# Kernel tuning notes

Measured on AMD Instinct MI355X. Metric: run time of the kernel, lower is better.

The kernel has to match this reference:

```python
import jax, jax.numpy as jnp
import numpy as np

NEG_INF = -jnp.inf


def setup_inputs() -> dict:
    B, T, D = 2, 512, 256
    key = jax.random.key(0)
    ks = jax.random.split(key, 12)
    inp = {
        'x': jax.random.normal(ks[0], (B, T, D), jnp.float32),
        'last_x': jnp.zeros((B, 1, D), jnp.float32),
        'last_num': jnp.zeros((B, 1, D), jnp.float32),
        'last_den': jnp.zeros((B, 1, D), jnp.float32),
        'time_decay': jax.random.normal(ks[1], (D,), jnp.float32) * 0.5,
        'time_first': jax.random.normal(ks[2], (D,), jnp.float32) * 0.5,
        'time_mix_k': jax.random.uniform(ks[3], (1, 1, D), jnp.float32),
        'time_mix_v': jax.random.uniform(ks[4], (1, 1, D), jnp.float32),
        'time_mix_r': jax.random.uniform(ks[5], (1, 1, D), jnp.float32),
        'Wk': jax.random.normal(ks[6], (D, D), jnp.float32) * 0.02,
        'Wv': jax.random.normal(ks[7], (D, D), jnp.float32) * 0.02,
        'Wr': jax.random.normal(ks[8], (D, D), jnp.float32) * 0.02,
        'Wo': jax.random.normal(ks[9], (D, D), jnp.float32) * 0.02,
    }
    return inp


def reference(x, last_x, last_num, last_den, time_decay, time_first,
              time_mix_k, time_mix_v, time_mix_r, Wk, Wv, Wr, Wo):
    B, T, D = x.shape

    # time_shift: prepend last_x, drop last step
    xs = jnp.concatenate([last_x, x[:, :-1, :]], axis=1)  # (B,T,D)

    k = (x * time_mix_k + xs * (1.0 - time_mix_k)) @ Wk.T
    v = (x * time_mix_v + xs * (1.0 - time_mix_v)) @ Wv.T
    r = (x * time_mix_r + xs * (1.0 - time_mix_r)) @ Wr.T
    sr = jax.nn.sigmoid(r)

    # --- run_wkv (quadratic exp-masked formulation, faithful to source) ---
    w = -jnp.exp(time_decay)                      # (D,)
    t = jnp.arange(T + 1, dtype=x.dtype)
    # wt[i, j] = j - i
    wt = t[None, :T] - t[:T, None]                # (T,T)
    tw = w[None, :] * t[1:, None]                 # (T,D): w * (j+1)
    twt = w[None, None, :] * wt[:, :, None]       # (T,T,D)
    # causal mask: -inf where j < i (strictly lower triangle, tril_(-1))
    ii = jnp.arange(T)
    mask = jnp.where(ii[:, None] > ii[None, :], NEG_INF, 0.0).astype(x.dtype)
    ktw = twt[None] + k[:, :, None, :] + mask[None, :, :, None]  # (B,T,T,D)
    etw = jnp.exp(tw)                             # (T,D)
    ektw = jnp.exp(ktw)                           # (B,T,T,D)
    num = etw[None] * last_num + jnp.einsum('bijd,bid->bjd', ektw, v)  # (B,T,D)
    den = etw[None] * last_den + ektw.sum(axis=1)                      # (B,T,D)
    num_prev = jnp.concatenate([last_num, num[:, :-1, :]], axis=1)
    den_prev = jnp.concatenate([last_den, den[:, :-1, :]], axis=1)
    euk = jnp.exp(time_first[None, None, :] + k)
    wkv = (num_prev + euk * v) / (den_prev + euk)
    # ----------------------------------------------------------------------

    out = (wkv * sr) @ Wo.T
    return (out, x[:, -1:, :], num[:, -1:, :], den[:, -1:, :])
```

## Files before the change

### kernel.cpp

```cpp
#include <hip/hip_runtime.h>

#define TT 512
#define DD 256
#define BB 2
#define MM (BB*TT)
#define LCH 16
#define NCH (TT/LCH)

__global__ __launch_bounds__(128)
void gemm_mix_t(const float* __restrict__ X, const float* __restrict__ Xlast,
                const float* __restrict__ W0, const float* __restrict__ W1,
                const float* __restrict__ W2,
                const float* __restrict__ mx0, const float* __restrict__ mx1,
                const float* __restrict__ mx2,
                float* __restrict__ O0, float* __restrict__ O1,
                float* __restrict__ O2)
{
    const int mat = blockIdx.z;
    const float* W  = (mat == 0) ? W0  : (mat == 1) ? W1  : W2;
    const float* mx = (mat == 0) ? mx0 : (mat == 1) ? mx1 : mx2;
    float*       O  = (mat == 0) ? O0  : (mat == 1) ? O1  : O2;

    const int n0  = blockIdx.x * 32;
    const int m0  = blockIdx.y * 64;
    const int b   = m0 / TT;
    const int t0  = m0 % TT;
    const int tid = threadIdx.x;

    const int cc = (tid & 15) * 4;
    const int r8 = tid >> 4;
    const int tm = tid >> 3;
    const int tn = tid & 7;

    __shared__ float As[64][68];
    __shared__ float Bs[64][36];

    float acc[4][4] = {};

    for (int k0 = 0; k0 < DD; k0 += 64) {
        #pragma unroll
        for (int i = 0; i < 8; ++i) {
            const int rr  = r8 + i * 8;
            const int row = m0 + rr;
            const float4 xc = *(const float4*)&X[row * DD + k0 + cc];
            float4 xp;
            if (t0 + rr == 0) xp = *(const float4*)&Xlast[b * DD + k0 + cc];
            else              xp = *(const float4*)&X[(row - 1) * DD + k0 + cc];
            const float4 mv = *(const float4*)&mx[k0 + cc];
            As[cc + 0][rr] = xp.x + (xc.x - xp.x) * mv.x;
            As[cc + 1][rr] = xp.y + (xc.y - xp.y) * mv.y;
            As[cc + 2][rr] = xp.z + (xc.z - xp.z) * mv.z;
            As[cc + 3][rr] = xp.w + (xc.w - xp.w) * mv.w;
        }
        #pragma unroll
        for (int i = 0; i < 4; ++i) {
            const int rr = r8 + i * 8;
            const float4 wv = *(const float4*)&W[(n0 + rr) * DD + k0 + cc];
            Bs[cc + 0][rr] = wv.x;
            Bs[cc + 1][rr] = wv.y;
            Bs[cc + 2][rr] = wv.z;
            Bs[cc + 3][rr] = wv.w;
        }
        __syncthreads();
        #pragma unroll
        for (int kk = 0; kk < 64; ++kk) {
            const float4 a4 = *(const float4*)&As[kk][tm * 4];
            const float4 b4 = *(const float4*)&Bs[kk][tn * 4];
            const float am[4] = {a4.x, a4.y, a4.z, a4.w};
            const float bn[4] = {b4.x, b4.y, b4.z, b4.w};
            #pragma unroll
            for (int i = 0; i < 4; ++i)
                #pragma unroll
                for (int j = 0; j < 4; ++j)
                    acc[i][j] = fmaf(am[i], bn[j], acc[i][j]);
        }
        __syncthreads();
    }

    #pragma unroll
    for (int j = 0; j < 4; ++j) {
        const float4 o = make_float4(acc[0][j], acc[1][j], acc[2][j], acc[3][j]);
        *(float4*)&O[(size_t)(b * DD + n0 + tn * 4 + j) * TT + t0 + tm * 4] = o;
    }
}

__global__ __launch_bounds__(256)
void wkv_scan(const float* __restrict__ kT, const float* __restrict__ vT,
              const float* __restrict__ rT, const float* __restrict__ x,
              const float* __restrict__ last_num, const float* __restrict__ last_den,
              const float* __restrict__ time_decay, const float* __restrict__ time_first,
              float* __restrict__ yT, float* __restrict__ out)
{
    const int tid  = threadIdx.x;
    const int ch   = blockIdx.x * 8 + (tid >> 5);
    const int lane = tid & 31;
    const int b    = ch >> 8;
    const int d    = ch & (DD - 1);

    const float w  = -__expf(time_decay[d]);
    const float ew = __expf(w);
    const float eu = __expf(time_first[d]);

    const size_t base = (size_t)ch * TT + lane * LCH;
    float k_[LCH], v_[LCH], r_[LCH];
    #pragma unroll
    for (int i = 0; i < 4; ++i) {
        *(float4*)&k_[4 * i] = *(const float4*)(kT + base + 4 * i);
        *(float4*)&v_[4 * i] = *(const float4*)(vT + base + 4 * i);
        *(float4*)&r_[4 * i] = *(const float4*)(rT + base + 4 * i);
    }

    float ek[LCH], ekv[LCH], sr[LCH];
    #pragma unroll
    for (int i = 0; i < LCH; ++i) {
        ek[i]  = __expf(k_[i]);
        ekv[i] = ek[i] * v_[i];
        sr[i]  = __builtin_amdgcn_rcpf(1.0f + __expf(-r_[i]));
    }

    float A = __expf(w * (float)LCH);
    float Bn = 0.0f, Bd = 0.0f;
    #pragma unroll
    for (int i = 0; i < LCH; ++i) {
        Bn = fmaf(ew, Bn, ekv[i]);
        Bd = fmaf(ew, Bd, ek[i]);
    }

    #pragma unroll
    for (int s = 1; s < 32; s <<= 1) {
        const float Ax  = __shfl_up(A, s, 32);
        const float Bnx = __shfl_up(Bn, s, 32);
        const float Bdx = __shfl_up(Bd, s, 32);
        if (lane >= s) {
            Bn = fmaf(A, Bnx, Bn);
            Bd = fmaf(A, Bdx, Bd);
            A *= Ax;
        }
    }

    float Aex  = __shfl_up(A, 1, 32);
    float Bnex = __shfl_up(Bn, 1, 32);
    float Bdex = __shfl_up(Bd, 1, 32);
    if (lane == 0) { Aex = 1.0f; Bnex = 0.0f; Bdex = 0.0f; }
    float sn = fmaf(Aex, last_num[ch], Bnex);
    float sd = fmaf(Aex, last_den[ch], Bdex);

    float y_[LCH];
    #pragma unroll
    for (int i = 0; i < LCH; ++i) {
        const float euk = eu * ek[i];
        const float wkv = (sn + eu * ekv[i]) * __builtin_amdgcn_rcpf(sd + euk);
        y_[i] = wkv * sr[i];
        sn = fmaf(ew, sn, ekv[i]);
        sd = fmaf(ew, sd, ek[i]);
    }
    #pragma unroll
    for (int i = 0; i < 4; ++i)
        *(float4*)(yT + base + 4 * i) = *(const float4*)&y_[4 * i];

    if (lane == 31) {
        out[MM * DD + BB * DD + ch]     = sn;
        out[MM * DD + 2 * BB * DD + ch] = sd;
    }
    if (lane == 0)
        out[MM * DD + ch] = x[(b * TT + TT - 1) * DD + d];
}

__global__ __launch_bounds__(64)
void gemm_out(const float* __restrict__ yT, const float* __restrict__ Wo,
              float* __restrict__ O)
{
    const int n0  = blockIdx.x * 32;
    const int m0  = blockIdx.y * 32;
    const int b   = m0 >> 9;
    const int t0  = m0 & (TT - 1);
    const int tid = threadIdx.x;

    __shared__ float As[64][36];
    __shared__ float Bs[64][36];

    const int tm = tid >> 3;
    const int tn = tid & 7;

    float acc[4][4] = {};

    for (int k0 = 0; k0 < DD; k0 += 64) {
        {
            const int mq = (tid & 7) * 4;
            #pragma unroll
            for (int i = 0; i < 8; ++i) {
                const int kk = (tid >> 3) + i * 8;
                *(float4*)&As[kk][mq] =
                    *(const float4*)&yT[(size_t)(b * DD + k0 + kk) * TT + t0 + mq];
            }
        }
        {
            const int cc = (tid & 15) * 4;
            #pragma unroll
            for (int i = 0; i < 8; ++i) {
                const int rr = (tid >> 4) + i * 4;
                const float4 wv = *(const float4*)&Wo[(n0 + rr) * DD + k0 + cc];
                Bs[cc + 0][rr] = wv.x;
                Bs[cc + 1][rr] = wv.y;
                Bs[cc + 2][rr] = wv.z;
                Bs[cc + 3][rr] = wv.w;
            }
        }
        __syncthreads();
        #pragma unroll
        for (int kk = 0; kk < 64; ++kk) {
            const float4 a4 = *(const float4*)&As[kk][tm * 4];
            const float4 b4 = *(const float4*)&Bs[kk][tn * 4];
            const float am[4] = {a4.x, a4.y, a4.z, a4.w};
            const float bn[4] = {b4.x, b4.y, b4.z, b4.w};
            #pragma unroll
            for (int i = 0; i < 4; ++i)
                #pragma unroll
                for (int j = 0; j < 4; ++j)
                    acc[i][j] = fmaf(am[i], bn[j], acc[i][j]);
        }
        __syncthreads();
    }

    #pragma unroll
    for (int i = 0; i < 4; ++i) {
        const float4 o = make_float4(acc[i][0], acc[i][1], acc[i][2], acc[i][3]);
        *(float4*)&O[(size_t)(m0 + tm * 4 + i) * DD + n0 + tn * 4] = o;
    }
}

extern "C" void kernel_launch(void* const* d_in, const int* in_sizes, int n_in,
                              void* d_out, int out_size, void* d_ws, size_t ws_size,
                              hipStream_t stream)
{
    const float* x    = (const float*)d_in[0];
    const float* lx   = (const float*)d_in[1];
    const float* lnum = (const float*)d_in[2];
    const float* lden = (const float*)d_in[3];
    const float* td   = (const float*)d_in[4];
    const float* tf   = (const float*)d_in[5];
    const float* mk   = (const float*)d_in[6];
    const float* mv   = (const float*)d_in[7];
    const float* mr   = (const float*)d_in[8];
    const float* Wk   = (const float*)d_in[9];
    const float* Wv   = (const float*)d_in[10];
    const float* Wr   = (const float*)d_in[11];
    const float* Wo   = (const float*)d_in[12];
    float* out = (float*)d_out;

    float* kT = (float*)d_ws;
    float* vT = kT + MM * DD;
    float* rT = vT + MM * DD;
    float* yT = rT + MM * DD;

    gemm_mix_t<<<dim3(8, 16, 3), 128, 0, stream>>>(
        x, lx, Wk, Wv, Wr, mk, mv, mr, kT, vT, rT);

    wkv_scan<<<dim3(64), 256, 0, stream>>>(
        kT, vT, rT, x, lnum, lden, td, tf, yT, out);

    gemm_out<<<dim3(8, 32), 64, 0, stream>>>(yT, Wo, out);
}
```

Baseline: 110.3 us.

## Double-buffer GEMM tiles with register prefetch and widen the WKV scan to 64 lanes

Both GEMM kernels now use double-buffered shared-memory tiles, prefetching the next K chunk into registers while the current one is computed, which removes one barrier per iteration. Blocks grow to 256 threads: the mix GEMM uses 64x64 tiles and the output GEMM gives each thread a 2x2 tile. The WKV scan uses full 64-lane wavefronts with 8-element chunks per lane and twice as many blocks, aiming for more parallelism and occupancy. The costs are a longer shuffle scan, fewer blocks in the mix GEMM, and lower per-thread compute density in the output GEMM.

```diff
diff --git a/kernel.cpp b/kernel.cpp
--- a/kernel.cpp
+++ b/kernel.cpp
@@ -4,10 +4,10 @@
 #define DD 256
 #define BB 2
 #define MM (BB*TT)
-#define LCH 16
+#define LCH 8
 #define NCH (TT/LCH)
 
-__global__ __launch_bounds__(128)
+__global__ __launch_bounds__(256)
 void gemm_mix_t(const float* __restrict__ X, const float* __restrict__ Xlast,
                 const float* __restrict__ W0, const float* __restrict__ W1,
                 const float* __restrict__ W2,
@@ -21,51 +21,71 @@
     const float* mx = (mat == 0) ? mx0 : (mat == 1) ? mx1 : mx2;
     float*       O  = (mat == 0) ? O0  : (mat == 1) ? O1  : O2;
 
-    const int n0  = blockIdx.x * 32;
+    const int n0  = blockIdx.x * 64;
     const int m0  = blockIdx.y * 64;
     const int b   = m0 / TT;
     const int t0  = m0 % TT;
     const int tid = threadIdx.x;
 
-    const int cc = (tid & 15) * 4;
-    const int r8 = tid >> 4;
-    const int tm = tid >> 3;
-    const int tn = tid & 7;
-
-    __shared__ float As[64][68];
-    __shared__ float Bs[64][36];
-
-    float acc[4][4] = {};
-
-    for (int k0 = 0; k0 < DD; k0 += 64) {
-        #pragma unroll
-        for (int i = 0; i < 8; ++i) {
-            const int rr  = r8 + i * 8;
+    const int cc = (tid & 7) * 4;
+    const int r8 = tid >> 3;
+    const int tm = tid >> 4;
+    const int tn = tid & 15;
+
+    __shared__ float As[2][32][68];
+    __shared__ float Bs[2][32][68];
+
+    float4 a0, a1, b0, b1;
+
+    auto load_chunk = [&](int k0) {
+        const float4 mv = *(const float4*)&mx[k0 + cc];
+        {
+            const int rr  = r8;
             const int row = m0 + rr;
-            const float4 xc = *(const float4*)&X[row * DD + k0 + cc];
+            const float4 xc = *(const float4*)&X[(size_t)row * DD + k0 + cc];
             float4 xp;
             if (t0 + rr == 0) xp = *(const float4*)&Xlast[b * DD + k0 + cc];
-            else              xp = *(const float4*)&X[(row - 1) * DD + k0 + cc];
-            const float4 mv = *(const float4*)&mx[k0 + cc];
-            As[cc + 0][rr] = xp.x + (xc.x - xp.x) * mv.x;
-            As[cc + 1][rr] = xp.y + (xc.y - xp.y) * mv.y;
-            As[cc + 2][rr] = xp.z + (xc.z - xp.z) * mv.z;
-            As[cc + 3][rr] = xp.w + (xc.w - xp.w) * mv.w;
-        }
-        #pragma unroll
-        for (int i = 0; i < 4; ++i) {
-            const int rr = r8 + i * 8;
-            const float4 wv = *(const float4*)&W[(n0 + rr) * DD + k0 + cc];
-            Bs[cc + 0][rr] = wv.x;
-            Bs[cc + 1][rr] = wv.y;
-            Bs[cc + 2][rr] = wv.z;
-            Bs[cc + 3][rr] = wv.w;
-        }
+            else              xp = *(const float4*)&X[(size_t)(row - 1) * DD + k0 + cc];
+            a0.x = xp.x + (xc.x - xp.x) * mv.x;
+            a0.y = xp.y + (xc.y - xp.y) * mv.y;
+            a0.z = xp.z + (xc.z - xp.z) * mv.z;
+            a0.w = xp.w + (xc.w - xp.w) * mv.w;
+            b0 = *(const float4*)&W[(size_t)(n0 + rr) * DD + k0 + cc];
+        }
+        {
+            const int rr  = r8 + 32;
+            const int row = m0 + rr;
+            const float4 xc = *(const float4*)&X[(size_t)row * DD + k0 + cc];
+            float4 xp;
+            if (t0 + rr == 0) xp = *(const float4*)&Xlast[b * DD + k0 + cc];
+            else              xp = *(const float4*)&X[(size_t)(row - 1) * DD + k0 + cc];
+            a1.x = xp.x + (xc.x - xp.x) * mv.x;
+            a1.y = xp.y + (xc.y - xp.y) * mv.y;
+            a1.z = xp.z + (xc.z - xp.z) * mv.z;
+            a1.w = xp.w + (xc.w - xp.w) * mv.w;
+            b1 = *(const float4*)&W[(size_t)(n0 + rr) * DD + k0 + cc];
+        }
+    };
+
+    float acc[4][4] = {};
+    load_chunk(0);
+
+    for (int c = 0; c < 8; ++c) {
+        const int buf = c & 1;
+        As[buf][cc + 0][r8]      = a0.x; As[buf][cc + 1][r8]      = a0.y;
+        As[buf][cc + 2][r8]      = a0.z; As[buf][cc + 3][r8]      = a0.w;
+        As[buf][cc + 0][r8 + 32] = a1.x; As[buf][cc + 1][r8 + 32] = a1.y;
+        As[buf][cc + 2][r8 + 32] = a1.z; As[buf][cc + 3][r8 + 32] = a1.w;
+        Bs[buf][cc + 0][r8]      = b0.x; Bs[buf][cc + 1][r8]      = b0.y;
+        Bs[buf][cc + 2][r8]      = b0.z; Bs[buf][cc + 3][r8]      = b0.w;
+        Bs[buf][cc + 0][r8 + 32] = b1.x; Bs[buf][cc + 1][r8 + 32] = b1.y;
+        Bs[buf][cc + 2][r8 + 32] = b1.z; Bs[buf][cc + 3][r8 + 32] = b1.w;
+        if (c < 7) load_chunk((c + 1) * 32);
         __syncthreads();
         #pragma unroll
-        for (int kk = 0; kk < 64; ++kk) {
-            const float4 a4 = *(const float4*)&As[kk][tm * 4];
-            const float4 b4 = *(const float4*)&Bs[kk][tn * 4];
+        for (int kk = 0; kk < 32; ++kk) {
+            const float4 a4 = *(const float4*)&As[buf][kk][tm * 4];
+            const float4 b4 = *(const float4*)&Bs[buf][kk][tn * 4];
             const float am[4] = {a4.x, a4.y, a4.z, a4.w};
             const float bn[4] = {b4.x, b4.y, b4.z, b4.w};
             #pragma unroll
@@ -74,7 +94,6 @@
                 for (int j = 0; j < 4; ++j)
                     acc[i][j] = fmaf(am[i], bn[j], acc[i][j]);
         }
-        __syncthreads();
     }
 
     #pragma unroll
@@ -92,8 +111,8 @@
               float* __restrict__ yT, float* __restrict__ out)
 {
     const int tid  = threadIdx.x;
-    const int ch   = blockIdx.x * 8 + (tid >> 5);
-    const int lane = tid & 31;
+    const int ch   = blockIdx.x * 4 + (tid >> 6);
+    const int lane = tid & 63;
     const int b    = ch >> 8;
     const int d    = ch & (DD - 1);
 
@@ -104,7 +123,7 @@
     const size_t base = (size_t)ch * TT + lane * LCH;
     float k_[LCH], v_[LCH], r_[LCH];
     #pragma unroll
-    for (int i = 0; i < 4; ++i) {
+    for (int i = 0; i < LCH / 4; ++i) {
         *(float4*)&k_[4 * i] = *(const float4*)(kT + base + 4 * i);
         *(float4*)&v_[4 * i] = *(const float4*)(vT + base + 4 * i);
         *(float4*)&r_[4 * i] = *(const float4*)(rT + base + 4 * i);
@@ -127,10 +146,10 @@
     }
 
     #pragma unroll
-    for (int s = 1; s < 32; s <<= 1) {
-        const float Ax  = __shfl_up(A, s, 32);
-        const float Bnx = __shfl_up(Bn, s, 32);
-        const float Bdx = __shfl_up(Bd, s, 32);
+    for (int s = 1; s < 64; s <<= 1) {
+        const float Ax  = __shfl_up(A, s, 64);
+        const float Bnx = __shfl_up(Bn, s, 64);
+        const float Bdx = __shfl_up(Bd, s, 64);
         if (lane >= s) {
             Bn = fmaf(A, Bnx, Bn);
             Bd = fmaf(A, Bdx, Bd);
@@ -138,9 +157,9 @@
         }
     }
 
-    float Aex  = __shfl_up(A, 1, 32);
-    float Bnex = __shfl_up(Bn, 1, 32);
-    float Bdex = __shfl_up(Bd, 1, 32);
+    float Aex  = __shfl_up(A, 1, 64);
+    float Bnex = __shfl_up(Bn, 1, 64);
+    float Bdex = __shfl_up(Bd, 1, 64);
     if (lane == 0) { Aex = 1.0f; Bnex = 0.0f; Bdex = 0.0f; }
     float sn = fmaf(Aex, last_num[ch], Bnex);
     float sd = fmaf(Aex, last_den[ch], Bdex);
@@ -155,10 +174,10 @@
         sd = fmaf(ew, sd, ek[i]);
     }
     #pragma unroll
-    for (int i = 0; i < 4; ++i)
+    for (int i = 0; i < LCH / 4; ++i)
         *(float4*)(yT + base + 4 * i) = *(const float4*)&y_[4 * i];
 
-    if (lane == 31) {
+    if (lane == 63) {
         out[MM * DD + BB * DD + ch]     = sn;
         out[MM * DD + 2 * BB * DD + ch] = sd;
     }
@@ -166,7 +185,7 @@
         out[MM * DD + ch] = x[(b * TT + TT - 1) * DD + d];
 }
 
-__global__ __launch_bounds__(64)
+__global__ __launch_bounds__(256)
 void gemm_out(const float* __restrict__ yT, const float* __restrict__ Wo,
               float* __restrict__ O)
 {
@@ -176,56 +195,53 @@
     const int t0  = m0 & (TT - 1);
     const int tid = threadIdx.x;
 
-    __shared__ float As[64][36];
-    __shared__ float Bs[64][36];
-
-    const int tm = tid >> 3;
-    const int tn = tid & 7;
-
-    float acc[4][4] = {};
-
-    for (int k0 = 0; k0 < DD; k0 += 64) {
-        {
-            const int mq = (tid & 7) * 4;
-            #pragma unroll
-            for (int i = 0; i < 8; ++i) {
-                const int kk = (tid >> 3) + i * 8;
-                *(float4*)&As[kk][mq] =
-                    *(const float4*)&yT[(size_t)(b * DD + k0 + kk) * TT + t0 + mq];
-            }
-        }
-        {
-            const int cc = (tid & 15) * 4;
-            #pragma unroll
-            for (int i = 0; i < 8; ++i) {
-                const int rr = (tid >> 4) + i * 4;
-                const float4 wv = *(const float4*)&Wo[(n0 + rr) * DD + k0 + cc];
-                Bs[cc + 0][rr] = wv.x;
-                Bs[cc + 1][rr] = wv.y;
-                Bs[cc + 2][rr] = wv.z;
-                Bs[cc + 3][rr] = wv.w;
-            }
-        }
+    __shared__ float As[2][64][36];
+    __shared__ float Bs[2][64][36];
+
+    const int tm = tid >> 4;
+    const int tn = tid & 15;
+
+    const int kq  = tid >> 3;
+    const int mq  = (tid & 7) * 4;
+    const int cc  = (tid & 15) * 4;
+    const int r16 = tid >> 4;
+
+    float4 av0, av1, wv0, wv1;
+    auto load_chunk = [&](int k0) {
+        av0 = *(const float4*)&yT[(size_t)(b * DD + k0 + kq) * TT + t0 + mq];
+        av1 = *(const float4*)&yT[(size_t)(b * DD + k0 + kq + 32) * TT + t0 + mq];
+        wv0 = *(const float4*)&Wo[(size_t)(n0 + r16) * DD + k0 + cc];
+        wv1 = *(const float4*)&Wo[(size_t)(n0 + r16 + 16) * DD + k0 + cc];
+    };
+
+    float acc[2][2] = {};
+    load_chunk(0);
+
+    for (int c = 0; c < 4; ++c) {
+        const int buf = c & 1;
+        *(float4*)&As[buf][kq][mq]      = av0;
+        *(float4*)&As[buf][kq + 32][mq] = av1;
+        Bs[buf][cc + 0][r16]      = wv0.x; Bs[buf][cc + 1][r16]      = wv0.y;
+        Bs[buf][cc + 2][r16]      = wv0.z; Bs[buf][cc + 3][r16]      = wv0.w;
+        Bs[buf][cc + 0][r16 + 16] = wv1.x; Bs[buf][cc + 1][r16 + 16] = wv1.y;
+        Bs[buf][cc + 2][r16 + 16] = wv1.z; Bs[buf][cc + 3][r16 + 16] = wv1.w;
+        if (c < 3) load_chunk((c + 1) * 64);
         __syncthreads();
         #pragma unroll
         for (int kk = 0; kk < 64; ++kk) {
-            const float4 a4 = *(const float4*)&As[kk][tm * 4];
-            const float4 b4 = *(const float4*)&Bs[kk][tn * 4];
-            const float am[4] = {a4.x, a4.y, a4.z, a4.w};
-            const float bn[4] = {b4.x, b4.y, b4.z, b4.w};
-            #pragma unroll
-            for (int i = 0; i < 4; ++i)
-                #pragma unroll
-                for (int j = 0; j < 4; ++j)
-                    acc[i][j] = fmaf(am[i], bn[j], acc[i][j]);
-        }
-        __syncthreads();
-    }
-
-    #pragma unroll
-    for (int i = 0; i < 4; ++i) {
-        const float4 o = make_float4(acc[i][0], acc[i][1], acc[i][2], acc[i][3]);
-        *(float4*)&O[(size_t)(m0 + tm * 4 + i) * DD + n0 + tn * 4] = o;
+            const float2 a2 = *(const float2*)&As[buf][kk][tm * 2];
+            const float2 b2 = *(const float2*)&Bs[buf][kk][tn * 2];
+            acc[0][0] = fmaf(a2.x, b2.x, acc[0][0]);
+            acc[0][1] = fmaf(a2.x, b2.y, acc[0][1]);
+            acc[1][0] = fmaf(a2.y, b2.x, acc[1][0]);
+            acc[1][1] = fmaf(a2.y, b2.y, acc[1][1]);
+        }
+    }
+
+    #pragma unroll
+    for (int i = 0; i < 2; ++i) {
+        const float2 o = make_float2(acc[i][0], acc[i][1]);
+        *(float2*)&O[(size_t)(m0 + tm * 2 + i) * DD + n0 + tn * 2] = o;
     }
 }
 
@@ -253,11 +269,11 @@
     float* rT = vT + MM * DD;
     float* yT = rT + MM * DD;
 
-    gemm_mix_t<<<dim3(8, 16, 3), 128, 0, stream>>>(
+    gemm_mix_t<<<dim3(4, 16, 3), 256, 0, stream>>>(
         x, lx, Wk, Wv, Wr, mk, mv, mr, kT, vT, rT);
 
-    wkv_scan<<<dim3(64), 256, 0, stream>>>(
+    wkv_scan<<<dim3(128), 256, 0, stream>>>(
         kT, vT, rT, x, lnum, lden, td, tf, yT, out);
 
-    gemm_out<<<dim3(8, 32), 64, 0, stream>>>(yT, Wo, out);
-}
+    gemm_out<<<dim3(8, 32), 256, 0, stream>>>(yT, Wo, out);
+}
```

Measured after the change: 102.2 us. 7.3% less time.

## Use single-wave blocks, split-K and finer scan chunks to spread work across CUs

Applied to the files above, without the earlier changes.

The mix GEMM now uses one 64-lane wave per block with 32x32 tiles and double-buffered shared memory. It prefetches the next K chunk into registers and drops the block barriers, which works because a single wave executes in lockstep. The output GEMM splits K across two waves and reduces their partial sums through shared memory. The WKV scan uses 8-element chunks with a full 64-lane wave scan, which gives four times as many blocks. Together these raise the number of blocks in flight on a small problem and cut barrier stalls, at the cost of more shuffle steps and an extra reduction pass.

```diff
diff --git a/kernel.cpp b/kernel.cpp
--- a/kernel.cpp
+++ b/kernel.cpp
@@ -4,10 +4,9 @@
 #define DD 256
 #define BB 2
 #define MM (BB*TT)
-#define LCH 16
-#define NCH (TT/LCH)
-
-__global__ __launch_bounds__(128)
+#define LCH 8
+
+__global__ __launch_bounds__(64)
 void gemm_mix_t(const float* __restrict__ X, const float* __restrict__ Xlast,
                 const float* __restrict__ W0, const float* __restrict__ W1,
                 const float* __restrict__ W2,
@@ -21,51 +20,58 @@
     const float* mx = (mat == 0) ? mx0 : (mat == 1) ? mx1 : mx2;
     float*       O  = (mat == 0) ? O0  : (mat == 1) ? O1  : O2;
 
-    const int n0  = blockIdx.x * 32;
-    const int m0  = blockIdx.y * 64;
-    const int b   = m0 / TT;
-    const int t0  = m0 % TT;
-    const int tid = threadIdx.x;
-
-    const int cc = (tid & 15) * 4;
-    const int r8 = tid >> 4;
-    const int tm = tid >> 3;
-    const int tn = tid & 7;
-
-    __shared__ float As[64][68];
-    __shared__ float Bs[64][36];
-
-    float acc[4][4] = {};
-
-    for (int k0 = 0; k0 < DD; k0 += 64) {
-        #pragma unroll
-        for (int i = 0; i < 8; ++i) {
-            const int rr  = r8 + i * 8;
+    const int n0   = blockIdx.x * 32;
+    const int m0   = blockIdx.y * 32;
+    const int b    = m0 / TT;
+    const int t0   = m0 % TT;
+    const int lane = threadIdx.x;
+
+    const int cc = (lane & 7) * 4;
+    const int g  = lane >> 3;
+    const int tm = lane >> 3;
+    const int tn = lane & 7;
+
+    __shared__ float As[2][32][36];
+    __shared__ float Bs[2][32][36];
+
+    float4 a[4], w4[4];
+
+    auto load_chunk = [&](int k0) {
+        const float4 mv = *(const float4*)&mx[k0 + cc];
+        #pragma unroll
+        for (int i = 0; i < 4; ++i) {
+            const int rr  = g + 8 * i;
             const int row = m0 + rr;
-            const float4 xc = *(const float4*)&X[row * DD + k0 + cc];
+            const float4 xc = *(const float4*)&X[(size_t)row * DD + k0 + cc];
             float4 xp;
             if (t0 + rr == 0) xp = *(const float4*)&Xlast[b * DD + k0 + cc];
-            else              xp = *(const float4*)&X[(row - 1) * DD + k0 + cc];
-            const float4 mv = *(const float4*)&mx[k0 + cc];
-            As[cc + 0][rr] = xp.x + (xc.x - xp.x) * mv.x;
-            As[cc + 1][rr] = xp.y + (xc.y - xp.y) * mv.y;
-            As[cc + 2][rr] = xp.z + (xc.z - xp.z) * mv.z;
-            As[cc + 3][rr] = xp.w + (xc.w - xp.w) * mv.w;
-        }
-        #pragma unroll
-        for (int i = 0; i < 4; ++i) {
-            const int rr = r8 + i * 8;
-            const float4 wv = *(const float4*)&W[(n0 + rr) * DD + k0 + cc];
-            Bs[cc + 0][rr] = wv.x;
-            Bs[cc + 1][rr] = wv.y;
-            Bs[cc + 2][rr] = wv.z;
-            Bs[cc + 3][rr] = wv.w;
-        }
-        __syncthreads();
-        #pragma unroll
-        for (int kk = 0; kk < 64; ++kk) {
-            const float4 a4 = *(const float4*)&As[kk][tm * 4];
-            const float4 b4 = *(const float4*)&Bs[kk][tn * 4];
+            else              xp = *(const float4*)&X[(size_t)(row - 1) * DD + k0 + cc];
+            a[i].x = xp.x + (xc.x - xp.x) * mv.x;
+            a[i].y = xp.y + (xc.y - xp.y) * mv.y;
+            a[i].z = xp.z + (xc.z - xp.z) * mv.z;
+            a[i].w = xp.w + (xc.w - xp.w) * mv.w;
+            w4[i] = *(const float4*)&W[(size_t)(n0 + rr) * DD + k0 + cc];
+        }
+    };
+
+    float acc[4][4] = {};
+    load_chunk(0);
+
+    for (int c = 0; c < 8; ++c) {
+        const int buf = c & 1;
+        #pragma unroll
+        for (int i = 0; i < 4; ++i) {
+            const int rr = g + 8 * i;
+            As[buf][cc + 0][rr] = a[i].x; As[buf][cc + 1][rr] = a[i].y;
+            As[buf][cc + 2][rr] = a[i].z; As[buf][cc + 3][rr] = a[i].w;
+            Bs[buf][cc + 0][rr] = w4[i].x; Bs[buf][cc + 1][rr] = w4[i].y;
+            Bs[buf][cc + 2][rr] = w4[i].z; Bs[buf][cc + 3][rr] = w4[i].w;
+        }
+        if (c < 7) load_chunk((c + 1) * 32);
+        #pragma unroll
+        for (int kk = 0; kk < 32; ++kk) {
+            const float4 a4 = *(const float4*)&As[buf][kk][tm * 4];
+            const float4 b4 = *(const float4*)&Bs[buf][kk][tn * 4];
             const float am[4] = {a4.x, a4.y, a4.z, a4.w};
             const float bn[4] = {b4.x, b4.y, b4.z, b4.w};
             #pragma unroll
@@ -74,7 +80,6 @@
                 for (int j = 0; j < 4; ++j)
                     acc[i][j] = fmaf(am[i], bn[j], acc[i][j]);
         }
-        __syncthreads();
     }
 
     #pragma unroll
@@ -84,7 +89,7 @@
     }
 }
 
-__global__ __launch_bounds__(256)
+__global__ __launch_bounds__(128)
 void wkv_scan(const float* __restrict__ kT, const float* __restrict__ vT,
               const float* __restrict__ rT, const float* __restrict__ x,
               const float* __restrict__ last_num, const float* __restrict__ last_den,
@@ -92,8 +97,8 @@
               float* __restrict__ yT, float* __restrict__ out)
 {
     const int tid  = threadIdx.x;
-    const int ch   = blockIdx.x * 8 + (tid >> 5);
-    const int lane = tid & 31;
+    const int ch   = blockIdx.x * 2 + (tid >> 6);
+    const int lane = tid & 63;
     const int b    = ch >> 8;
     const int d    = ch & (DD - 1);
 
@@ -104,7 +109,7 @@
     const size_t base = (size_t)ch * TT + lane * LCH;
     float k_[LCH], v_[LCH], r_[LCH];
     #pragma unroll
-    for (int i = 0; i < 4; ++i) {
+    for (int i = 0; i < LCH / 4; ++i) {
         *(float4*)&k_[4 * i] = *(const float4*)(kT + base + 4 * i);
         *(float4*)&v_[4 * i] = *(const float4*)(vT + base + 4 * i);
         *(float4*)&r_[4 * i] = *(const float4*)(rT + base + 4 * i);
@@ -127,10 +132,10 @@
     }
 
     #pragma unroll
-    for (int s = 1; s < 32; s <<= 1) {
-        const float Ax  = __shfl_up(A, s, 32);
-        const float Bnx = __shfl_up(Bn, s, 32);
-        const float Bdx = __shfl_up(Bd, s, 32);
+    for (int s = 1; s < 64; s <<= 1) {
+        const float Ax  = __shfl_up(A, s, 64);
+        const float Bnx = __shfl_up(Bn, s, 64);
+        const float Bdx = __shfl_up(Bd, s, 64);
         if (lane >= s) {
             Bn = fmaf(A, Bnx, Bn);
             Bd = fmaf(A, Bdx, Bd);
@@ -138,9 +143,9 @@
         }
     }
 
-    float Aex  = __shfl_up(A, 1, 32);
-    float Bnex = __shfl_up(Bn, 1, 32);
-    float Bdex = __shfl_up(Bd, 1, 32);
+    float Aex  = __shfl_up(A, 1, 64);
+    float Bnex = __shfl_up(Bn, 1, 64);
+    float Bdex = __shfl_up(Bd, 1, 64);
     if (lane == 0) { Aex = 1.0f; Bnex = 0.0f; Bdex = 0.0f; }
     float sn = fmaf(Aex, last_num[ch], Bnex);
     float sd = fmaf(Aex, last_den[ch], Bdex);
@@ -155,10 +160,10 @@
         sd = fmaf(ew, sd, ek[i]);
     }
     #pragma unroll
-    for (int i = 0; i < 4; ++i)
+    for (int i = 0; i < LCH / 4; ++i)
         *(float4*)(yT + base + 4 * i) = *(const float4*)&y_[4 * i];
 
-    if (lane == 31) {
+    if (lane == 63) {
         out[MM * DD + BB * DD + ch]     = sn;
         out[MM * DD + 2 * BB * DD + ch] = sd;
     }
@@ -166,51 +171,58 @@
         out[MM * DD + ch] = x[(b * TT + TT - 1) * DD + d];
 }
 
-__global__ __launch_bounds__(64)
+__global__ __launch_bounds__(128)
 void gemm_out(const float* __restrict__ yT, const float* __restrict__ Wo,
               float* __restrict__ O)
 {
-    const int n0  = blockIdx.x * 32;
-    const int m0  = blockIdx.y * 32;
-    const int b   = m0 >> 9;
-    const int t0  = m0 & (TT - 1);
-    const int tid = threadIdx.x;
-
-    __shared__ float As[64][36];
-    __shared__ float Bs[64][36];
-
-    const int tm = tid >> 3;
-    const int tn = tid & 7;
+    const int n0   = blockIdx.x * 32;
+    const int m0   = blockIdx.y * 32;
+    const int b    = m0 >> 9;
+    const int t0   = m0 & (TT - 1);
+    const int tid  = threadIdx.x;
+    const int wv   = tid >> 6;
+    const int lane = tid & 63;
+
+    __shared__ float As[2][32][40];
+    __shared__ float Bs[2][32][36];
+
+    const int tm = lane >> 3;
+    const int tn = lane & 7;
+    const int kr = lane >> 3;
+    const int mq = (lane & 7) * 4;
+    const int cc = (lane & 7) * 4;
+    const int g  = lane >> 3;
+
+    const int kbase = wv * 128;
+
+    float4 av[4], wv4[4];
+    auto load_chunk = [&](int k0) {
+        #pragma unroll
+        for (int i = 0; i < 4; ++i)
+            av[i] = *(const float4*)&yT[(size_t)(b * DD + k0 + kr + 8 * i) * TT + t0 + mq];
+        #pragma unroll
+        for (int i = 0; i < 4; ++i)
+            wv4[i] = *(const float4*)&Wo[(size_t)(n0 + g + 8 * i) * DD + k0 + cc];
+    };
 
     float acc[4][4] = {};
-
-    for (int k0 = 0; k0 < DD; k0 += 64) {
-        {
-            const int mq = (tid & 7) * 4;
-            #pragma unroll
-            for (int i = 0; i < 8; ++i) {
-                const int kk = (tid >> 3) + i * 8;
-                *(float4*)&As[kk][mq] =
-                    *(const float4*)&yT[(size_t)(b * DD + k0 + kk) * TT + t0 + mq];
-            }
-        }
-        {
-            const int cc = (tid & 15) * 4;
-            #pragma unroll
-            for (int i = 0; i < 8; ++i) {
-                const int rr = (tid >> 4) + i * 4;
-                const float4 wv = *(const float4*)&Wo[(n0 + rr) * DD + k0 + cc];
-                Bs[cc + 0][rr] = wv.x;
-                Bs[cc + 1][rr] = wv.y;
-                Bs[cc + 2][rr] = wv.z;
-                Bs[cc + 3][rr] = wv.w;
-            }
-        }
-        __syncthreads();
-        #pragma unroll
-        for (int kk = 0; kk < 64; ++kk) {
-            const float4 a4 = *(const float4*)&As[kk][tm * 4];
-            const float4 b4 = *(const float4*)&Bs[kk][tn * 4];
+    load_chunk(kbase);
+
+    for (int c = 0; c < 4; ++c) {
+        #pragma unroll
+        for (int i = 0; i < 4; ++i)
+            *(float4*)&As[wv][kr + 8 * i][mq] = av[i];
+        #pragma unroll
+        for (int i = 0; i < 4; ++i) {
+            const int rr = g + 8 * i;
+            Bs[wv][cc + 0][rr] = wv4[i].x; Bs[wv][cc + 1][rr] = wv4[i].y;
+            Bs[wv][cc + 2][rr] = wv4[i].z; Bs[wv][cc + 3][rr] = wv4[i].w;
+        }
+        if (c < 3) load_chunk(kbase + (c + 1) * 32);
+        #pragma unroll
+        for (int kk = 0; kk < 32; ++kk) {
+            const float4 a4 = *(const float4*)&As[wv][kk][tm * 4];
+            const float4 b4 = *(const float4*)&Bs[wv][kk][tn * 4];
             const float am[4] = {a4.x, a4.y, a4.z, a4.w};
             const float bn[4] = {b4.x, b4.y, b4.z, b4.w};
             #pragma unroll
@@ -219,13 +231,27 @@
                 for (int j = 0; j < 4; ++j)
                     acc[i][j] = fmaf(am[i], bn[j], acc[i][j]);
         }
-        __syncthreads();
-    }
-
-    #pragma unroll
-    for (int i = 0; i < 4; ++i) {
-        const float4 o = make_float4(acc[i][0], acc[i][1], acc[i][2], acc[i][3]);
-        *(float4*)&O[(size_t)(m0 + tm * 4 + i) * DD + n0 + tn * 4] = o;
+    }
+
+    float* red = &As[1][0][0];
+    if (wv == 1) {
+        #pragma unroll
+        for (int i = 0; i < 4; ++i)
+            *(float4*)&red[lane * 20 + i * 4] =
+                make_float4(acc[i][0], acc[i][1], acc[i][2], acc[i][3]);
+    }
+    __syncthreads();
+    if (wv == 0) {
+        #pragma unroll
+        for (int i = 0; i < 4; ++i) {
+            const float4 o = *(const float4*)&red[lane * 20 + i * 4];
+            acc[i][0] += o.x; acc[i][1] += o.y;
+            acc[i][2] += o.z; acc[i][3] += o.w;
+        }
+        #pragma unroll
+        for (int i = 0; i < 4; ++i)
+            *(float4*)&O[(size_t)(m0 + tm * 4 + i) * DD + n0 + tn * 4] =
+                make_float4(acc[i][0], acc[i][1], acc[i][2], acc[i][3]);
     }
 }
 
@@ -253,11 +279,11 @@
     float* rT = vT + MM * DD;
     float* yT = rT + MM * DD;
 
-    gemm_mix_t<<<dim3(8, 16, 3), 128, 0, stream>>>(
+    gemm_mix_t<<<dim3(8, 32, 3), 64, 0, stream>>>(
         x, lx, Wk, Wv, Wr, mk, mv, mr, kT, vT, rT);
 
-    wkv_scan<<<dim3(64), 256, 0, stream>>>(
+    wkv_scan<<<dim3(256), 128, 0, stream>>>(
         kT, vT, rT, x, lnum, lden, td, tf, yT, out);
 
-    gemm_out<<<dim3(8, 32), 64, 0, stream>>>(yT, Wo, out);
-}
+    gemm_out<<<dim3(8, 32), 128, 0, stream>>>(yT, Wo, out);
+}
```

After: 101.3 us. 8.2% less time.
